# Kernel tuning notes

Hardware: AMD Instinct MI355X
Metric: run time of the kernel (lower is better)

The kernel has to match this reference:

```python
import jax, jax.numpy as jnp
import numpy as np
import math

D_MODEL = 1024
NUM_HEADS = 16
D_KV = 64
INNER = NUM_HEADS * D_KV
NUM_BUCKETS = 32
MAX_DISTANCE = 128


def _relative_position_bucket(relative_position, num_buckets=NUM_BUCKETS, max_distance=MAX_DISTANCE):
    # bidirectional T5 bucketing
    n = -relative_position
    num_buckets = num_buckets // 2
    ret = (n < 0).astype(jnp.int32) * num_buckets
    n = jnp.abs(n)
    max_exact = num_buckets // 2
    is_small = n < max_exact
    n_safe = jnp.maximum(n, 1).astype(jnp.float32)  # avoid log(0); masked by is_small
    val_if_large = max_exact + (
        jnp.log(n_safe / max_exact) / math.log(max_distance / max_exact) * (num_buckets - max_exact)
    ).astype(jnp.int32)
    val_if_large = jnp.minimum(val_if_large, num_buckets - 1)
    return jnp.where(is_small, n, val_if_large) + ret


def _position_bias(rel_emb, q_len, k_len):
    ctx = jnp.arange(q_len)[:, None]
    mem = jnp.arange(k_len)[None, :]
    buckets = _relative_position_bucket(mem - ctx)          # [q, k]
    values = rel_emb[buckets]                               # [q, k, H]
    return jnp.transpose(values, (2, 0, 1))[None]           # [1, H, q, k]


def setup_inputs() -> dict:
    key = jax.random.key(0)
    ks = jax.random.split(key, 6)
    B, S = 2, 2048
    scale = 1.0 / math.sqrt(D_MODEL)
    return {
        "hidden_states": jax.random.normal(ks[0], (B, S, D_MODEL), dtype=jnp.float32),
        "mask": jnp.zeros((B, 1, 1, S), dtype=jnp.float32),
        "Wq": jax.random.normal(ks[1], (D_MODEL, INNER), dtype=jnp.float32) * scale,
        "Wk": jax.random.normal(ks[2], (D_MODEL, INNER), dtype=jnp.float32) * scale,
        "Wv": jax.random.normal(ks[3], (D_MODEL, INNER), dtype=jnp.float32) * scale,
        "Wo": jax.random.normal(ks[4], (INNER, D_MODEL), dtype=jnp.float32) * scale,
        "rel_emb": jax.random.normal(ks[5], (NUM_BUCKETS, NUM_HEADS), dtype=jnp.float32),
    }


def reference(hidden_states, mask, Wq, Wk, Wv, Wo, rel_emb):
    B, S, _ = hidden_states.shape
    def split_heads(x):
        return jnp.transpose(x.reshape(B, -1, NUM_HEADS, D_KV), (0, 2, 1, 3))  # [B,H,S,d]
    q = split_heads(hidden_states @ Wq)
    k = split_heads(hidden_states @ Wk)
    v = split_heads(hidden_states @ Wv)
    scores = jnp.einsum("bhqd,bhkd->bhqk", q, k)            # unscaled, T5-style
    position_bias = _position_bias(rel_emb, S, S)           # [1,H,S,S]
    scores = scores + position_bias + mask
    attn = jax.nn.softmax(scores, axis=-1)
    context = jnp.einsum("bhqk,bhkd->bhqd", attn, v)
    context = jnp.transpose(context, (0, 2, 1, 3)).reshape(B, S, INNER)
    output = context @ Wo
    return output, position_bias
```

## Files before the change

### kernel.cpp

```cpp
#include <hip/hip_runtime.h>
#include <cstdint>

#define AS1 __attribute__((address_space(1)))
#define AS3 __attribute__((address_space(3)))

typedef _Float16 half8 __attribute__((ext_vector_type(8)));
typedef _Float16 half4_t __attribute__((ext_vector_type(4)));
typedef float v4f __attribute__((ext_vector_type(4)));

__device__ __forceinline__ void async_ld16(const void* g, void* l) {
  __builtin_amdgcn_global_load_lds((const AS1 uint32_t*)g, (AS3 uint32_t*)l, 16, 0, 0);
}

__device__ __forceinline__ int t5_bucket(int delta) {
  int n = -delta;
  int ret = 0;
  if (n < 0) { ret = 16; n = -n; }
  if (n < 8) return n + ret;
  if (n >= 91) return 15 + ret;
  if ((n & (n - 1)) == 0) {
    int l = 31 - __clz(n);
    int v = 2 + 2 * l;
    return (v > 15 ? 15 : v) + ret;
  }
  int v = 8 + (int)(logf((float)n * 0.125f) * (8.0f / logf(16.0f)));
  return (v > 15 ? 15 : v) + ret;
}

__global__ void k_cvt(const float* __restrict__ src, _Float16* __restrict__ dst) {
  int t = blockIdx.x * 256 + threadIdx.x;
  float4 f = ((const float4*)src)[t];
  half4_t h = {(_Float16)f.x, (_Float16)f.y, (_Float16)f.z, (_Float16)f.w};
  ((half4_t*)dst)[t] = h;
}

__global__ void k_wt_all(const float* __restrict__ Wq, const float* __restrict__ Wk,
                         const float* __restrict__ Wv, const float* __restrict__ Wo,
                         _Float16* __restrict__ wqkvT, _Float16* __restrict__ woT) {
  __shared__ float tile[32][33];
  const int z = blockIdx.z;
  const float* src = (z == 0) ? Wq : (z == 1) ? Wk : (z == 2) ? Wv : Wo;
  _Float16* dst = (z < 3) ? (wqkvT + ((size_t)z << 20)) : woT;
  int tx = threadIdx.x, ty = threadIdx.y;
  int bx = blockIdx.x * 32, by = blockIdx.y * 32;
#pragma unroll
  for (int i = 0; i < 32; i += 8)
    tile[ty + i][tx] = src[(size_t)(by + ty + i) * 1024 + bx + tx];
  __syncthreads();
#pragma unroll
  for (int i = 0; i < 32; i += 8)
    dst[(size_t)(bx + ty + i) * 1024 + by + tx] = (_Float16)tile[tx][ty + i];
}

template <bool F16OUT>
__global__ __launch_bounds__(256, 2) void k_gemm(const _Float16* __restrict__ A,
                                                 const _Float16* __restrict__ BT,
                                                 void* __restrict__ Cv,
                                                 _Float16* __restrict__ vT, int K, int ldc) {
  __shared__ __align__(16) _Float16 As[128 * 32];
  __shared__ __align__(16) _Float16 Bs[128 * 32];
  const int tid = threadIdx.x;
  const int wave = tid >> 6, lane = tid & 63;
  const int l15 = lane & 15, quad = lane >> 4;
  const int m0 = blockIdx.y * 128, n0 = blockIdx.x * 128;
  const int wm = (wave >> 1) * 64, wn = (wave & 1) * 64;
  const int r0 = tid >> 2, c0 = (tid & 3) * 8;
  v4f acc[4][4] = {};
  for (int k0 = 0; k0 < K; k0 += 32) {
    __syncthreads();
    async_ld16(A + (size_t)(m0 + r0) * K + k0 + c0, (char*)As + (size_t)(wave * 64) * 16);
    async_ld16(A + (size_t)(m0 + 64 + r0) * K + k0 + c0,
               (char*)As + (size_t)(256 + wave * 64) * 16);
    async_ld16(BT + (size_t)(n0 + r0) * K + k0 + c0, (char*)Bs + (size_t)(wave * 64) * 16);
    async_ld16(BT + (size_t)(n0 + 64 + r0) * K + k0 + c0,
               (char*)Bs + (size_t)(256 + wave * 64) * 16);
    __syncthreads();
    half8 af[4], bf[4];
#pragma unroll
    for (int mt = 0; mt < 4; ++mt)
      af[mt] = *(const half8*)(As + (wm + mt * 16 + l15) * 32 + quad * 8);
#pragma unroll
    for (int nt = 0; nt < 4; ++nt)
      bf[nt] = *(const half8*)(Bs + (wn + nt * 16 + l15) * 32 + quad * 8);
#pragma unroll
    for (int mt = 0; mt < 4; ++mt)
#pragma unroll
      for (int nt = 0; nt < 4; ++nt)
        acc[mt][nt] = __builtin_amdgcn_mfma_f32_16x16x32_f16(af[mt], bf[nt], acc[mt][nt], 0, 0, 0);
  }
  if (F16OUT && n0 >= 2048) {
#pragma unroll
    for (int mt = 0; mt < 4; ++mt)
#pragma unroll
      for (int nt = 0; nt < 4; ++nt) {
        int col = n0 + wn + nt * 16 + l15 - 2048;
        int row0 = m0 + wm + mt * 16 + quad * 4;
        int bb = row0 >> 11, s0 = row0 & 2047;
        half4_t hv = {(_Float16)acc[mt][nt][0], (_Float16)acc[mt][nt][1],
                      (_Float16)acc[mt][nt][2], (_Float16)acc[mt][nt][3]};
        *(half4_t*)(vT + ((size_t)bb * 1024 + col) * 2048 + s0) = hv;
      }
    return;
  }
#pragma unroll
  for (int mt = 0; mt < 4; ++mt)
#pragma unroll
    for (int nt = 0; nt < 4; ++nt)
#pragma unroll
      for (int r = 0; r < 4; ++r) {
        int row = m0 + wm + mt * 16 + quad * 4 + r;
        int col = n0 + wn + nt * 16 + l15;
        if (F16OUT)
          ((_Float16*)Cv)[(size_t)row * ldc + col] = (_Float16)acc[mt][nt][r];
        else
          ((float*)Cv)[(size_t)row * ldc + col] = acc[mt][nt][r];
      }
}

__global__ __launch_bounds__(256, 2) void k_gemm_n64(const _Float16* __restrict__ A,
                                                     const _Float16* __restrict__ BT,
                                                     float* __restrict__ C, int K, int ldc) {
  __shared__ __align__(16) _Float16 As[128 * 32];
  __shared__ __align__(16) _Float16 Bs[64 * 32];
  const int tid = threadIdx.x;
  const int wave = tid >> 6, lane = tid & 63;
  const int l15 = lane & 15, quad = lane >> 4;
  const int m0 = blockIdx.y * 128, n0 = blockIdx.x * 64;
  const int wm = (wave >> 1) * 64, wn = (wave & 1) * 32;
  const int r0 = tid >> 2, c0 = (tid & 3) * 8;
  v4f acc[4][2] = {};
  for (int k0 = 0; k0 < K; k0 += 32) {
    __syncthreads();
    async_ld16(A + (size_t)(m0 + r0) * K + k0 + c0, (char*)As + (size_t)(wave * 64) * 16);
    async_ld16(A + (size_t)(m0 + 64 + r0) * K + k0 + c0,
               (char*)As + (size_t)(256 + wave * 64) * 16);
    async_ld16(BT + (size_t)(n0 + r0) * K + k0 + c0, (char*)Bs + (size_t)(wave * 64) * 16);
    __syncthreads();
    half8 af[4], bf[2];
#pragma unroll
    for (int mt = 0; mt < 4; ++mt)
      af[mt] = *(const half8*)(As + (wm + mt * 16 + l15) * 32 + quad * 8);
#pragma unroll
    for (int nt = 0; nt < 2; ++nt)
      bf[nt] = *(const half8*)(Bs + (wn + nt * 16 + l15) * 32 + quad * 8);
#pragma unroll
    for (int mt = 0; mt < 4; ++mt)
#pragma unroll
      for (int nt = 0; nt < 2; ++nt)
        acc[mt][nt] = __builtin_amdgcn_mfma_f32_16x16x32_f16(af[mt], bf[nt], acc[mt][nt], 0, 0, 0);
  }
#pragma unroll
  for (int mt = 0; mt < 4; ++mt)
#pragma unroll
    for (int nt = 0; nt < 2; ++nt)
#pragma unroll
      for (int r = 0; r < 4; ++r)
        C[(size_t)(m0 + wm + mt * 16 + quad * 4 + r) * ldc + n0 + wn + nt * 16 + l15] =
            acc[mt][nt][r];
}

__global__ __launch_bounds__(256, 3) void k_attn_bias(const _Float16* __restrict__ qkv,
                                                      const _Float16* __restrict__ vT,
                                                      const float* __restrict__ mask,
                                                      const float* __restrict__ rel,
                                                      _Float16* __restrict__ ctx,
                                                      float* __restrict__ outb) {
  constexpr int S = 2048, LD = 3072;
  __shared__ __align__(16) _Float16 Ks[64 * 72];
  __shared__ __align__(16) _Float16 VT[64 * 72];
  __shared__ __align__(16) _Float16 Psh[128 * 72];
  __shared__ float btab[512];
  const int tid = threadIdx.x, wave = tid >> 6, lane = tid & 63;
  const int l15 = lane & 15, quad = lane >> 4;
  const int h = blockIdx.y, b = blockIdx.z;

  for (int j = tid; j < 512; j += 256) btab[j] = rel[t5_bucket(j - 256) * 16 + h];
  const float c_past = rel[15 * 16 + h];
  const float c_fut = rel[31 * 16 + h];
  __syncthreads();

  if (blockIdx.x >= 16) {
    const int blk = blockIdx.x - 16;
    float4* op = (float4*)outb + (size_t)h * 2048 * 512;
#pragma unroll 4
    for (int i = 0; i < 256; ++i) {
      int idx = blk * 65536 + i * 256 + tid;
      int k4 = idx & 511;
      int q = b * 1024 + (idx >> 9);
      int kb = k4 * 4;
      float4 v;
      if (kb - q >= 91) {
        v = make_float4(c_fut, c_fut, c_fut, c_fut);
      } else if (q - kb - 3 >= 91) {
        v = make_float4(c_past, c_past, c_past, c_past);
      } else {
        v.x = btab[kb + 0 - q + 256];
        v.y = btab[kb + 1 - q + 256];
        v.z = btab[kb + 2 - q + 256];
        v.w = btab[kb + 3 - q + 256];
      }
      op[(size_t)q * 512 + k4] = v;
    }
    return;
  }

  const int q0 = blockIdx.x * 128;

  half8 bq[2][2];
#pragma unroll
  for (int qt = 0; qt < 2; ++qt) {
    const _Float16* qp = qkv + (size_t)(b * S + q0 + wave * 32 + qt * 16 + l15) * LD + h * 64;
    bq[qt][0] = *(const half8*)(qp + quad * 8);
    bq[qt][1] = *(const half8*)(qp + 32 + quad * 8);
  }
  v4f o[2][4] = {};
  float mrun[2] = {-INFINITY, -INFINITY};
  float lrun[2] = {0.f, 0.f};

  const int srow = tid >> 2, scol = (tid & 3) * 8;
  const _Float16* kg = qkv + (size_t)(b * S + srow) * LD + 1024 + h * 64 + scol;
  const _Float16* vg = vT + ((size_t)((b * 16 + h) * 64 + srow)) * S + scol;
  const float4* mkp = (const float4*)(mask + (size_t)b * S);

  for (int kv0 = 0; kv0 < S; kv0 += 64) {
    half8 kr0 = *(const half8*)(kg + (size_t)kv0 * LD);
    half8 kr1 = *(const half8*)(kg + (size_t)kv0 * LD + 32);
    half8 vr0 = *(const half8*)(vg + kv0);
    half8 vr1 = *(const half8*)(vg + kv0 + 32);
    float4 mk[4];
#pragma unroll
    for (int mt = 0; mt < 4; ++mt) mk[mt] = mkp[(kv0 >> 2) + mt * 4 + quad];
    __syncthreads();
    *(half8*)(Ks + srow * 72 + scol) = kr0;
    *(half8*)(Ks + srow * 72 + scol + 32) = kr1;
    *(half8*)(VT + srow * 72 + scol) = vr0;
    *(half8*)(VT + srow * 72 + scol + 32) = vr1;
    __syncthreads();

    v4f sc[2][4] = {};
#pragma unroll
    for (int kc = 0; kc < 2; ++kc)
#pragma unroll
      for (int mt = 0; mt < 4; ++mt) {
        half8 af = *(const half8*)(Ks + (mt * 16 + l15) * 72 + kc * 32 + quad * 8);
        sc[0][mt] = __builtin_amdgcn_mfma_f32_16x16x32_f16(af, bq[0][kc], sc[0][mt], 0, 0, 0);
        sc[1][mt] = __builtin_amdgcn_mfma_f32_16x16x32_f16(af, bq[1][kc], sc[1][mt], 0, 0, 0);
      }

    const int diff = kv0 - q0;
    const bool mixed = (diff >= -153) && (diff <= 217);
    const float cf = (diff >= 218) ? c_fut : c_past;
    v4f cm[4];
#pragma unroll
    for (int mt = 0; mt < 4; ++mt) {
      cm[mt][0] = mk[mt].x; cm[mt][1] = mk[mt].y; cm[mt][2] = mk[mt].z; cm[mt][3] = mk[mt].w;
      if (!mixed) {
        cm[mt][0] += cf; cm[mt][1] += cf; cm[mt][2] += cf; cm[mt][3] += cf;
      }
    }
    if (mixed) {
#pragma unroll
      for (int qt = 0; qt < 2; ++qt) {
        const int qq = q0 + wave * 32 + qt * 16 + l15;
#pragma unroll
        for (int mt = 0; mt < 4; ++mt) {
          int base = kv0 + mt * 16 + quad * 4 - qq + 256;
#pragma unroll
          for (int r = 0; r < 4; ++r) sc[qt][mt][r] += btab[base + r] + cm[mt][r];
        }
      }
    } else {
#pragma unroll
      for (int qt = 0; qt < 2; ++qt)
#pragma unroll
        for (int mt = 0; mt < 4; ++mt)
#pragma unroll
          for (int r = 0; r < 4; ++r) sc[qt][mt][r] += cm[mt][r];
    }

#pragma unroll
    for (int qt = 0; qt < 2; ++qt) {
      v4f m4 = sc[qt][0];
#pragma unroll
      for (int r = 0; r < 4; ++r) {
        m4[r] = fmaxf(m4[r], sc[qt][1][r]);
        m4[r] = fmaxf(m4[r], sc[qt][2][r]);
        m4[r] = fmaxf(m4[r], sc[qt][3][r]);
      }
      float mx = fmaxf(fmaxf(m4[0], m4[1]), fmaxf(m4[2], m4[3]));
      mx = fmaxf(mx, __shfl_xor(mx, 16, 64));
      mx = fmaxf(mx, __shfl_xor(mx, 32, 64));
      float mnew = fmaxf(mrun[qt], mx);
      float alpha = __expf(mrun[qt] - mnew);
      mrun[qt] = mnew;
      v4f s4 = {};
#pragma unroll
      for (int mt = 0; mt < 4; ++mt)
#pragma unroll
        for (int r = 0; r < 4; ++r) {
          float p = __expf(sc[qt][mt][r] - mnew);
          sc[qt][mt][r] = p;
          s4[r] += p;
        }
      float rs = (s4[0] + s4[1]) + (s4[2] + s4[3]);
      rs += __shfl_xor(rs, 16, 64);
      rs += __shfl_xor(rs, 32, 64);
      lrun[qt] = lrun[qt] * alpha + rs;
#pragma unroll
      for (int dt = 0; dt < 4; ++dt)
#pragma unroll
        for (int r = 0; r < 4; ++r) o[qt][dt][r] *= alpha;
      const int prow = wave * 32 + qt * 16 + l15;
#pragma unroll
      for (int mt = 0; mt < 4; ++mt) {
        half4_t ph = {(_Float16)sc[qt][mt][0], (_Float16)sc[qt][mt][1],
                      (_Float16)sc[qt][mt][2], (_Float16)sc[qt][mt][3]};
        *(half4_t*)(Psh + prow * 72 + mt * 16 + quad * 4) = ph;
      }
    }
    __syncthreads();

#pragma unroll
    for (int kc = 0; kc < 2; ++kc) {
      half8 bp0 = *(const half8*)(Psh + (wave * 32 + l15) * 72 + kc * 32 + quad * 8);
      half8 bp1 = *(const half8*)(Psh + (wave * 32 + 16 + l15) * 72 + kc * 32 + quad * 8);
#pragma unroll
      for (int dt = 0; dt < 4; ++dt) {
        half8 av = *(const half8*)(VT + (dt * 16 + l15) * 72 + kc * 32 + quad * 8);
        o[0][dt] = __builtin_amdgcn_mfma_f32_16x16x32_f16(av, bp0, o[0][dt], 0, 0, 0);
        o[1][dt] = __builtin_amdgcn_mfma_f32_16x16x32_f16(av, bp1, o[1][dt], 0, 0, 0);
      }
    }
  }
#pragma unroll
  for (int qt = 0; qt < 2; ++qt) {
    float inv = 1.0f / lrun[qt];
    const size_t token = (size_t)(b * S + q0 + wave * 32 + qt * 16 + l15);
#pragma unroll
    for (int dt = 0; dt < 4; ++dt) {
      half4_t hv = {(_Float16)(o[qt][dt][0] * inv), (_Float16)(o[qt][dt][1] * inv),
                    (_Float16)(o[qt][dt][2] * inv), (_Float16)(o[qt][dt][3] * inv)};
      *(half4_t*)(ctx + token * 1024 + h * 64 + dt * 16 + quad * 4) = hv;
    }
  }
}

extern "C" void kernel_launch(void* const* d_in, const int* in_sizes, int n_in,
                              void* d_out, int out_size, void* d_ws, size_t ws_size,
                              hipStream_t stream) {
  const float* hs = (const float*)d_in[0];
  const float* mask = (const float*)d_in[1];
  const float* Wq = (const float*)d_in[2];
  const float* Wk = (const float*)d_in[3];
  const float* Wv = (const float*)d_in[4];
  const float* Wo = (const float*)d_in[5];
  const float* rel = (const float*)d_in[6];
  float* out = (float*)d_out;

  char* ws = (char*)d_ws;
  _Float16* hsF = (_Float16*)(ws);
  _Float16* wqkvT = (_Float16*)(ws + (8u << 20));
  _Float16* woT = (_Float16*)(ws + (14u << 20));
  _Float16* qkv = (_Float16*)(ws + (16u << 20));
  _Float16* ctx = (_Float16*)(ws + (40u << 20));
  _Float16* vT = (_Float16*)(ws + (48u << 20));

  k_cvt<<<4096, 256, 0, stream>>>(hs, hsF);
  k_wt_all<<<dim3(32, 32, 4), dim3(32, 8), 0, stream>>>(Wq, Wk, Wv, Wo, wqkvT, woT);

  k_gemm<true><<<dim3(24, 32), 256, 0, stream>>>(hsF, wqkvT, qkv, vT, 1024, 3072);
  k_attn_bias<<<dim3(24, 16, 2), 256, 0, stream>>>(qkv, vT, mask, rel, ctx, out + 4194304);
  k_gemm_n64<<<dim3(16, 32), 256, 0, stream>>>(ctx, woT, out, 1024, 1024);
}
```

Before: 436.9 us.

## Double attention query tile to 256 per block and drop P barrier

Each attention workgroup now handles 256 queries, 64 per wave, instead of 128. This halves the number of attention blocks and the K/V tile loads per query, and reuses each K/V LDS fragment across four query subtiles. The launch bound, bias table size and the mixed-region bounds are widened to match. The __syncthreads between writing P and the PV MFMA is removed, since each wave reads only its own P rows. The cost is more registers per thread and only 256 attention blocks in the grid, which lowers occupancy and latency hiding.

```diff
diff --git a/kernel.cpp b/kernel.cpp
--- a/kernel.cpp
+++ b/kernel.cpp
@@ -159,7 +159,7 @@
             acc[mt][nt][r];
 }
 
-__global__ __launch_bounds__(256, 3) void k_attn_bias(const _Float16* __restrict__ qkv,
+__global__ __launch_bounds__(256, 2) void k_attn_bias(const _Float16* __restrict__ qkv,
                                                       const _Float16* __restrict__ vT,
                                                       const float* __restrict__ mask,
                                                       const float* __restrict__ rel,
@@ -168,19 +168,19 @@
   constexpr int S = 2048, LD = 3072;
   __shared__ __align__(16) _Float16 Ks[64 * 72];
   __shared__ __align__(16) _Float16 VT[64 * 72];
-  __shared__ __align__(16) _Float16 Psh[128 * 72];
-  __shared__ float btab[512];
+  __shared__ __align__(16) _Float16 Psh[256 * 72];
+  __shared__ float btab[1024];
   const int tid = threadIdx.x, wave = tid >> 6, lane = tid & 63;
   const int l15 = lane & 15, quad = lane >> 4;
   const int h = blockIdx.y, b = blockIdx.z;
 
-  for (int j = tid; j < 512; j += 256) btab[j] = rel[t5_bucket(j - 256) * 16 + h];
+  for (int j = tid; j < 1024; j += 256) btab[j] = rel[t5_bucket(j - 512) * 16 + h];
   const float c_past = rel[15 * 16 + h];
   const float c_fut = rel[31 * 16 + h];
   __syncthreads();
 
-  if (blockIdx.x >= 16) {
-    const int blk = blockIdx.x - 16;
+  if (blockIdx.x >= 8) {
+    const int blk = blockIdx.x - 8;
     float4* op = (float4*)outb + (size_t)h * 2048 * 512;
 #pragma unroll 4
     for (int i = 0; i < 256; ++i) {
@@ -194,28 +194,29 @@
       } else if (q - kb - 3 >= 91) {
         v = make_float4(c_past, c_past, c_past, c_past);
       } else {
-        v.x = btab[kb + 0 - q + 256];
-        v.y = btab[kb + 1 - q + 256];
-        v.z = btab[kb + 2 - q + 256];
-        v.w = btab[kb + 3 - q + 256];
+        v.x = btab[kb + 0 - q + 512];
+        v.y = btab[kb + 1 - q + 512];
+        v.z = btab[kb + 2 - q + 512];
+        v.w = btab[kb + 3 - q + 512];
       }
       op[(size_t)q * 512 + k4] = v;
     }
     return;
   }
 
-  const int q0 = blockIdx.x * 128;
-
-  half8 bq[2][2];
-#pragma unroll
-  for (int qt = 0; qt < 2; ++qt) {
-    const _Float16* qp = qkv + (size_t)(b * S + q0 + wave * 32 + qt * 16 + l15) * LD + h * 64;
+  const int q0 = blockIdx.x * 256;
+  const int qbase = q0 + wave * 64;
+
+  half8 bq[4][2];
+#pragma unroll
+  for (int qt = 0; qt < 4; ++qt) {
+    const _Float16* qp = qkv + (size_t)(b * S + qbase + qt * 16 + l15) * LD + h * 64;
     bq[qt][0] = *(const half8*)(qp + quad * 8);
     bq[qt][1] = *(const half8*)(qp + 32 + quad * 8);
   }
-  v4f o[2][4] = {};
-  float mrun[2] = {-INFINITY, -INFINITY};
-  float lrun[2] = {0.f, 0.f};
+  v4f o[4][4] = {};
+  float mrun[4] = {-INFINITY, -INFINITY, -INFINITY, -INFINITY};
+  float lrun[4] = {0.f, 0.f, 0.f, 0.f};
 
   const int srow = tid >> 2, scol = (tid & 3) * 8;
   const _Float16* kg = qkv + (size_t)(b * S + srow) * LD + 1024 + h * 64 + scol;
@@ -237,19 +238,20 @@
     *(half8*)(VT + srow * 72 + scol + 32) = vr1;
     __syncthreads();
 
-    v4f sc[2][4] = {};
+    v4f sc[4][4] = {};
 #pragma unroll
     for (int kc = 0; kc < 2; ++kc)
 #pragma unroll
       for (int mt = 0; mt < 4; ++mt) {
         half8 af = *(const half8*)(Ks + (mt * 16 + l15) * 72 + kc * 32 + quad * 8);
-        sc[0][mt] = __builtin_amdgcn_mfma_f32_16x16x32_f16(af, bq[0][kc], sc[0][mt], 0, 0, 0);
-        sc[1][mt] = __builtin_amdgcn_mfma_f32_16x16x32_f16(af, bq[1][kc], sc[1][mt], 0, 0, 0);
+#pragma unroll
+        for (int qt = 0; qt < 4; ++qt)
+          sc[qt][mt] = __builtin_amdgcn_mfma_f32_16x16x32_f16(af, bq[qt][kc], sc[qt][mt], 0, 0, 0);
       }
 
     const int diff = kv0 - q0;
-    const bool mixed = (diff >= -153) && (diff <= 217);
-    const float cf = (diff >= 218) ? c_fut : c_past;
+    const bool mixed = (diff >= -153) && (diff <= 345);
+    const float cf = (diff > 345) ? c_fut : c_past;
     v4f cm[4];
 #pragma unroll
     for (int mt = 0; mt < 4; ++mt) {
@@ -260,18 +262,18 @@
     }
     if (mixed) {
 #pragma unroll
-      for (int qt = 0; qt < 2; ++qt) {
-        const int qq = q0 + wave * 32 + qt * 16 + l15;
+      for (int qt = 0; qt < 4; ++qt) {
+        const int qq = qbase + qt * 16 + l15;
 #pragma unroll
         for (int mt = 0; mt < 4; ++mt) {
-          int base = kv0 + mt * 16 + quad * 4 - qq + 256;
+          int base = kv0 + mt * 16 + quad * 4 - qq + 512;
 #pragma unroll
           for (int r = 0; r < 4; ++r) sc[qt][mt][r] += btab[base + r] + cm[mt][r];
         }
       }
     } else {
 #pragma unroll
-      for (int qt = 0; qt < 2; ++qt)
+      for (int qt = 0; qt < 4; ++qt)
 #pragma unroll
         for (int mt = 0; mt < 4; ++mt)
 #pragma unroll
@@ -279,7 +281,7 @@
     }
 
 #pragma unroll
-    for (int qt = 0; qt < 2; ++qt) {
+    for (int qt = 0; qt < 4; ++qt) {
       v4f m4 = sc[qt][0];
 #pragma unroll
       for (int r = 0; r < 4; ++r) {
@@ -310,7 +312,7 @@
       for (int dt = 0; dt < 4; ++dt)
 #pragma unroll
         for (int r = 0; r < 4; ++r) o[qt][dt][r] *= alpha;
-      const int prow = wave * 32 + qt * 16 + l15;
+      const int prow = wave * 64 + qt * 16 + l15;
 #pragma unroll
       for (int mt = 0; mt < 4; ++mt) {
         half4_t ph = {(_Float16)sc[qt][mt][0], (_Float16)sc[qt][mt][1],
@@ -318,24 +320,26 @@
         *(half4_t*)(Psh + prow * 72 + mt * 16 + quad * 4) = ph;
       }
     }
-    __syncthreads();
 
 #pragma unroll
     for (int kc = 0; kc < 2; ++kc) {
-      half8 bp0 = *(const half8*)(Psh + (wave * 32 + l15) * 72 + kc * 32 + quad * 8);
-      half8 bp1 = *(const half8*)(Psh + (wave * 32 + 16 + l15) * 72 + kc * 32 + quad * 8);
-#pragma unroll
-      for (int dt = 0; dt < 4; ++dt) {
-        half8 av = *(const half8*)(VT + (dt * 16 + l15) * 72 + kc * 32 + quad * 8);
-        o[0][dt] = __builtin_amdgcn_mfma_f32_16x16x32_f16(av, bp0, o[0][dt], 0, 0, 0);
-        o[1][dt] = __builtin_amdgcn_mfma_f32_16x16x32_f16(av, bp1, o[1][dt], 0, 0, 0);
-      }
-    }
-  }
-#pragma unroll
-  for (int qt = 0; qt < 2; ++qt) {
+      half8 av[4];
+#pragma unroll
+      for (int dt = 0; dt < 4; ++dt)
+        av[dt] = *(const half8*)(VT + (dt * 16 + l15) * 72 + kc * 32 + quad * 8);
+#pragma unroll
+      for (int qt = 0; qt < 4; ++qt) {
+        half8 bp = *(const half8*)(Psh + (wave * 64 + qt * 16 + l15) * 72 + kc * 32 + quad * 8);
+#pragma unroll
+        for (int dt = 0; dt < 4; ++dt)
+          o[qt][dt] = __builtin_amdgcn_mfma_f32_16x16x32_f16(av[dt], bp, o[qt][dt], 0, 0, 0);
+      }
+    }
+  }
+#pragma unroll
+  for (int qt = 0; qt < 4; ++qt) {
     float inv = 1.0f / lrun[qt];
-    const size_t token = (size_t)(b * S + q0 + wave * 32 + qt * 16 + l15);
+    const size_t token = (size_t)(b * S + qbase + qt * 16 + l15);
 #pragma unroll
     for (int dt = 0; dt < 4; ++dt) {
       half4_t hv = {(_Float16)(o[qt][dt][0] * inv), (_Float16)(o[qt][dt][1] * inv),
@@ -369,6 +373,6 @@
   k_wt_all<<<dim3(32, 32, 4), dim3(32, 8), 0, stream>>>(Wq, Wk, Wv, Wo, wqkvT, woT);
 
   k_gemm<true><<<dim3(24, 32), 256, 0, stream>>>(hsF, wqkvT, qkv, vT, 1024, 3072);
-  k_attn_bias<<<dim3(24, 16, 2), 256, 0, stream>>>(qkv, vT, mask, rel, ctx, out + 4194304);
+  k_attn_bias<<<dim3(16, 16, 2), 256, 0, stream>>>(qkv, vT, mask, rel, ctx, out + 4194304);
   k_gemm_n64<<<dim3(16, 32), 256, 0, stream>>>(ctx, woT, out, 1024, 1024);
 }
```

After: 483.0 us. 10.6% more time.

## Move position-bias writes into QKV GEMM and drop a barrier in attention

Applied to the files above, without the earlier changes.

The large position-bias tensor used to be written by extra blocks appended to the attention grid. It is now written by 512 of the QKV projection GEMM blocks, a few float4 stores per K iteration. The aim is to overlap the bandwidth-heavy bias stores with the compute-bound GEMM, and to let the attention kernel run only its compute blocks. The attention kernel also drops a block barrier between writing P to shared memory and the PV MFMAs, since each wave reads only its own rows. The trade-off is extra store traffic and register pressure inside the GEMM loop, plus a race risk if that barrier was protecting other shared memory.

```diff
diff --git a/kernel.cpp b/kernel.cpp
--- a/kernel.cpp
+++ b/kernel.cpp
@@ -52,19 +52,32 @@
     dst[(size_t)(bx + ty + i) * 1024 + by + tx] = (_Float16)tile[tx][ty + i];
 }
 
-template <bool F16OUT>
-__global__ __launch_bounds__(256, 2) void k_gemm(const _Float16* __restrict__ A,
-                                                 const _Float16* __restrict__ BT,
-                                                 void* __restrict__ Cv,
-                                                 _Float16* __restrict__ vT, int K, int ldc) {
+__global__ __launch_bounds__(256, 2) void k_gemm_qkv_bias(
+    const _Float16* __restrict__ A, const _Float16* __restrict__ BT,
+    _Float16* __restrict__ qkv, _Float16* __restrict__ vT,
+    const float* __restrict__ rel, float* __restrict__ outb) {
   __shared__ __align__(16) _Float16 As[128 * 32];
   __shared__ __align__(16) _Float16 Bs[128 * 32];
+  __shared__ float btab[256];
   const int tid = threadIdx.x;
   const int wave = tid >> 6, lane = tid & 63;
   const int l15 = lane & 15, quad = lane >> 4;
   const int m0 = blockIdx.y * 128, n0 = blockIdx.x * 128;
   const int wm = (wave >> 1) * 64, wn = (wave & 1) * 64;
   const int r0 = tid >> 2, c0 = (tid & 3) * 8;
+  constexpr int K = 1024;
+
+  const int bid = blockIdx.y * 24 + blockIdx.x;
+  const bool do_bias = bid < 512;
+  const int hB = bid >> 5;
+  const int qoff = (bid & 31) * 64;
+  float c_past = 0.f, c_fut = 0.f;
+  if (do_bias) {
+    btab[tid & 255] = rel[t5_bucket((tid & 255) - 128) * 16 + hB];
+    c_past = rel[15 * 16 + hB];
+    c_fut = rel[31 * 16 + hB];
+  }
+
   v4f acc[4][4] = {};
   for (int k0 = 0; k0 < K; k0 += 32) {
     __syncthreads();
@@ -75,6 +88,29 @@
     async_ld16(BT + (size_t)(n0 + 64 + r0) * K + k0 + c0,
                (char*)Bs + (size_t)(256 + wave * 64) * 16);
     __syncthreads();
+
+    if (do_bias) {
+      const int iter = k0 >> 5;
+#pragma unroll
+      for (int j = 0; j < 4; ++j) {
+        int fi = iter * 1024 + j * 256 + tid;
+        int qr = qoff + (fi >> 9);
+        int kb = (fi & 511) * 4;
+        float4 v;
+        if (kb - qr >= 91) {
+          v = make_float4(c_fut, c_fut, c_fut, c_fut);
+        } else if (qr - kb - 3 >= 91) {
+          v = make_float4(c_past, c_past, c_past, c_past);
+        } else {
+          v.x = btab[kb + 0 - qr + 128];
+          v.y = btab[kb + 1 - qr + 128];
+          v.z = btab[kb + 2 - qr + 128];
+          v.w = btab[kb + 3 - qr + 128];
+        }
+        ((float4*)outb)[(size_t)bid * 32768 + fi] = v;
+      }
+    }
+
     half8 af[4], bf[4];
 #pragma unroll
     for (int mt = 0; mt < 4; ++mt)
@@ -88,7 +124,7 @@
       for (int nt = 0; nt < 4; ++nt)
         acc[mt][nt] = __builtin_amdgcn_mfma_f32_16x16x32_f16(af[mt], bf[nt], acc[mt][nt], 0, 0, 0);
   }
-  if (F16OUT && n0 >= 2048) {
+  if (n0 >= 2048) {
 #pragma unroll
     for (int mt = 0; mt < 4; ++mt)
 #pragma unroll
@@ -107,14 +143,9 @@
 #pragma unroll
     for (int nt = 0; nt < 4; ++nt)
 #pragma unroll
-      for (int r = 0; r < 4; ++r) {
-        int row = m0 + wm + mt * 16 + quad * 4 + r;
-        int col = n0 + wn + nt * 16 + l15;
-        if (F16OUT)
-          ((_Float16*)Cv)[(size_t)row * ldc + col] = (_Float16)acc[mt][nt][r];
-        else
-          ((float*)Cv)[(size_t)row * ldc + col] = acc[mt][nt][r];
-      }
+      for (int r = 0; r < 4; ++r)
+        qkv[(size_t)(m0 + wm + mt * 16 + quad * 4 + r) * 3072 + n0 + wn + nt * 16 + l15] =
+            (_Float16)acc[mt][nt][r];
 }
 
 __global__ __launch_bounds__(256, 2) void k_gemm_n64(const _Float16* __restrict__ A,
@@ -159,12 +190,11 @@
             acc[mt][nt][r];
 }
 
-__global__ __launch_bounds__(256, 3) void k_attn_bias(const _Float16* __restrict__ qkv,
-                                                      const _Float16* __restrict__ vT,
-                                                      const float* __restrict__ mask,
-                                                      const float* __restrict__ rel,
-                                                      _Float16* __restrict__ ctx,
-                                                      float* __restrict__ outb) {
+__global__ __launch_bounds__(256, 3) void k_attn(const _Float16* __restrict__ qkv,
+                                                 const _Float16* __restrict__ vT,
+                                                 const float* __restrict__ mask,
+                                                 const float* __restrict__ rel,
+                                                 _Float16* __restrict__ ctx) {
   constexpr int S = 2048, LD = 3072;
   __shared__ __align__(16) _Float16 Ks[64 * 72];
   __shared__ __align__(16) _Float16 VT[64 * 72];
@@ -172,39 +202,11 @@
   __shared__ float btab[512];
   const int tid = threadIdx.x, wave = tid >> 6, lane = tid & 63;
   const int l15 = lane & 15, quad = lane >> 4;
-  const int h = blockIdx.y, b = blockIdx.z;
+  const int q0 = blockIdx.x * 128, h = blockIdx.y, b = blockIdx.z;
 
   for (int j = tid; j < 512; j += 256) btab[j] = rel[t5_bucket(j - 256) * 16 + h];
   const float c_past = rel[15 * 16 + h];
   const float c_fut = rel[31 * 16 + h];
-  __syncthreads();
-
-  if (blockIdx.x >= 16) {
-    const int blk = blockIdx.x - 16;
-    float4* op = (float4*)outb + (size_t)h * 2048 * 512;
-#pragma unroll 4
-    for (int i = 0; i < 256; ++i) {
-      int idx = blk * 65536 + i * 256 + tid;
-      int k4 = idx & 511;
-      int q = b * 1024 + (idx >> 9);
-      int kb = k4 * 4;
-      float4 v;
-      if (kb - q >= 91) {
-        v = make_float4(c_fut, c_fut, c_fut, c_fut);
-      } else if (q - kb - 3 >= 91) {
-        v = make_float4(c_past, c_past, c_past, c_past);
-      } else {
-        v.x = btab[kb + 0 - q + 256];
-        v.y = btab[kb + 1 - q + 256];
-        v.z = btab[kb + 2 - q + 256];
-        v.w = btab[kb + 3 - q + 256];
-      }
-      op[(size_t)q * 512 + k4] = v;
-    }
-    return;
-  }
-
-  const int q0 = blockIdx.x * 128;
 
   half8 bq[2][2];
 #pragma unroll
@@ -318,7 +320,6 @@
         *(half4_t*)(Psh + prow * 72 + mt * 16 + quad * 4) = ph;
       }
     }
-    __syncthreads();
 
 #pragma unroll
     for (int kc = 0; kc < 2; ++kc) {
@@ -368,7 +369,8 @@
   k_cvt<<<4096, 256, 0, stream>>>(hs, hsF);
   k_wt_all<<<dim3(32, 32, 4), dim3(32, 8), 0, stream>>>(Wq, Wk, Wv, Wo, wqkvT, woT);
 
-  k_gemm<true><<<dim3(24, 32), 256, 0, stream>>>(hsF, wqkvT, qkv, vT, 1024, 3072);
-  k_attn_bias<<<dim3(24, 16, 2), 256, 0, stream>>>(qkv, vT, mask, rel, ctx, out + 4194304);
+  k_gemm_qkv_bias<<<dim3(24, 32), 256, 0, stream>>>(hsF, wqkvT, qkv, vT, rel,
+                                                    out + 4194304);
+  k_attn<<<dim3(16, 16, 2), 256, 0, stream>>>(qkv, vT, mask, rel, ctx);
   k_gemm_n64<<<dim3(16, 32), 256, 0, stream>>>(ctx, woT, out, 1024, 1024);
 }
```

Result: no change. 435.2 us (-0.4%).
